# Performance work log

Hardware: AMD Instinct MI355X
Metric: run time of the kernel (lower is better)

Reference implementation:

```python
import jax, jax.numpy as jnp
import numpy as np

B, S, D_IN = 32, 4096, 256
D, T, NB, K = 256, 256, 4, 5  # d_model, compressed_len, n_blocks, kernel_size
EPS = 1e-5


def setup_inputs() -> dict:
    key = jax.random.key(0)
    ks = jax.random.split(key, 20)
    x = jax.random.normal(ks[0], (B, S, D_IN), jnp.float32)
    # ragged valid-prefix lengths in [1, S]
    lengths = jax.random.randint(ks[1], (B,), 1, S + 1)
    mask = jnp.arange(S)[None, :] < lengths[:, None]  # bool [B,S]
    sc = 0.02
    inp = {
        'x': x,
        'mask': mask,
        'in_w': jax.random.normal(ks[2], (D_IN, D), jnp.float32) * sc,
        'in_b': jnp.zeros((D,), jnp.float32),
        'ln_g': jnp.ones((NB, D), jnp.float32),
        'ln_b': jnp.zeros((NB, D), jnp.float32),
        'dw_w': jax.random.normal(ks[3], (NB, D, 1, K), jnp.float32) * sc,
        'dw_b': jnp.zeros((NB, D), jnp.float32),
        'win_w': jax.random.normal(ks[4], (NB, D, 2 * D), jnp.float32) * sc,
        'win_b': jnp.zeros((NB, 2 * D), jnp.float32),
        'wout_w': jax.random.normal(ks[5], (NB, D, D), jnp.float32) * sc,
        'wout_b': jnp.zeros((NB, D), jnp.float32),
        'fn_g': jnp.ones((D,), jnp.float32),
        'fn_b': jnp.zeros((D,), jnp.float32),
    }
    return inp


def layer_norm(h, g, b):
    mu = jnp.mean(h, axis=-1, keepdims=True)
    var = jnp.mean((h - mu) ** 2, axis=-1, keepdims=True)
    return (h - mu) * jax.lax.rsqrt(var + EPS) * g + b


def compress(x, mask, target_len):
    # Vectorized equivalent of the per-sample F.interpolate(mode='linear',
    # align_corners=False) loop: src = (j+0.5)*(L/T) - 0.5, clamped, lerp.
    lengths = mask.astype(jnp.int32).sum(axis=1)  # [B]
    Lf = lengths.astype(x.dtype)
    j = jnp.arange(target_len, dtype=x.dtype)
    src = (j[None, :] + 0.5) * (Lf[:, None] / target_len) - 0.5  # [B,T]
    src = jnp.clip(src, 0.0, jnp.maximum(Lf[:, None] - 1.0, 0.0))
    i0 = jnp.floor(src).astype(jnp.int32)
    i1 = jnp.minimum(i0 + 1, jnp.maximum(lengths[:, None] - 1, 0))
    w = (src - i0.astype(x.dtype))[..., None]  # [B,T,1]
    gather = jax.vmap(lambda xb, ib: xb[ib])  # [S,D],[T] -> [T,D]
    out = (1.0 - w) * gather(x, i0) + w * gather(x, i1)  # [B,T,D]
    valid = lengths > 0
    out = jnp.where(valid[:, None, None], out, 0.0)
    comp_mask = jnp.broadcast_to(valid[:, None], (x.shape[0], target_len))
    return out, comp_mask


def conv_block(h, g, b, dww, dwb, winw, winb, woutw, woutb):
    residual = h
    hn = layer_norm(h, g, b)
    hc = jax.lax.conv_general_dilated(
        hn.transpose(0, 2, 1), dww, window_strides=(1,),
        padding=[(K // 2, K // 2)], dimension_numbers=('NCW', 'OIW', 'NCW'),
        feature_group_count=D)
    hc = hc.transpose(0, 2, 1) + dwb  # [B,T,D]
    gv = hc @ winw + winb
    gate, val = jnp.split(gv, 2, axis=-1)
    h2 = jax.nn.sigmoid(gate) * jax.nn.gelu(val, approximate=False)
    return residual + h2 @ woutw + woutb


def reference(x, mask, in_w, in_b, ln_g, ln_b, dw_w, dw_b, win_w, win_b,
              wout_w, wout_b, fn_g, fn_b):
    xc, comp_mask = compress(x, mask, T)
    h = xc @ in_w + in_b
    for i in range(NB):
        h = conv_block(h, ln_g[i], ln_b[i], dw_w[i], dw_b[i], win_w[i],
                       win_b[i], wout_w[i], wout_b[i])
    return layer_norm(h, fn_g, fn_b), comp_mask
```

## Files before the change

kernel.cpp:

```cpp
#include <hip/hip_runtime.h>
#include <math.h>

#define B_    32
#define S_    4096
#define DIN_  256
#define D_    256
#define T_    256
#define NB_   4
#define K_    5
#define EPS_  1e-5f
#define ROWS_ (B_ * T_)

#define ORS_  16
#define CR_   32
#define BR_   36
#define SEGS_ 16
#define ASTR  264
#define HSTR  264

typedef short  shortx8  __attribute__((ext_vector_type(8)));
typedef float  floatx4  __attribute__((ext_vector_type(4)));
typedef float  floatx16 __attribute__((ext_vector_type(16)));

__device__ __forceinline__ unsigned short f2bf(float f) {
    unsigned int u = __float_as_uint(f);
    u += 0x7FFFu + ((u >> 16) & 1u);
    return (unsigned short)(u >> 16);
}
__device__ __forceinline__ float bf2f(unsigned short s) {
    return __uint_as_float((unsigned int)s << 16);
}
__device__ __forceinline__ unsigned int pack2bf(float a, float b) {
    return (unsigned int)f2bf(a) | ((unsigned int)f2bf(b) << 16);
}
__device__ __forceinline__ float bf2f_lo(unsigned int u) {
    return __uint_as_float(u << 16);
}
__device__ __forceinline__ float bf2f_hi(unsigned int u) {
    return __uint_as_float(u & 0xFFFF0000u);
}

__global__ void k_setup(const float* __restrict__ in_w, const float* __restrict__ win_w,
                        const float* __restrict__ wout_w, const unsigned int* __restrict__ mask_w,
                        unsigned short* __restrict__ wt_in, unsigned short* __restrict__ wt_in_lo,
                        unsigned short* __restrict__ wt_win,
                        unsigned short* __restrict__ wt_wout, int* __restrict__ lengths) {
    int z = blockIdx.z;
    int tid = threadIdx.x;

    if (z == 9) {
        int b = blockIdx.y * 16 + blockIdx.x;
        if (b >= B_) return;
        __shared__ int smode;
        if (tid < 64) {
            unsigned int w0 = mask_w[0];
            unsigned int vi = (tid < 32) ? mask_w[tid * 1024] : 0u;
            unsigned long long anyu8 = __ballot(vi > 1u);
            if (tid == 0) smode = (w0 == 0x3F800000u) ? 2 : (anyu8 ? 1 : 0);
        }
        __syncthreads();
        int mode = smode;
        int s = 0;
        if (mode == 0) {
            const int* m = (const int*)mask_w;
            for (int i = tid; i < S_; i += 256) s += (m[(size_t)b * S_ + i] != 0);
        } else if (mode == 2) {
            const float* m = (const float*)mask_w;
            for (int i = tid; i < S_; i += 256) s += (m[(size_t)b * S_ + i] != 0.0f);
        } else {
            const unsigned char* m = (const unsigned char*)mask_w;
            for (int i = tid; i < S_; i += 256) s += (m[(size_t)b * S_ + i] != 0);
        }
        __shared__ int sm[256];
        sm[tid] = s;
        __syncthreads();
        for (int off = 128; off > 0; off >>= 1) {
            if (tid < off) sm[tid] += sm[tid + off];
            __syncthreads();
        }
        if (tid == 0) lengths[b] = sm[0];
        return;
    }

    const float* src; unsigned short* dst; int N;
    if (z == 0)      { src = in_w;                                   dst = wt_in;                                   N = D_;     }
    else if (z <= 4) { src = win_w  + (size_t)(z - 1) * D_ * 2 * D_; dst = wt_win  + (size_t)(z - 1) * 2 * D_ * D_; N = 2 * D_; }
    else             { src = wout_w + (size_t)(z - 5) * D_ * D_;     dst = wt_wout + (size_t)(z - 5) * D_ * D_;     N = D_;     }
    int bx = blockIdx.x * 32;
    int by = blockIdx.y * 32;
    if (bx >= N) return;
    __shared__ float tile[32][33];
    int tx = tid & 31, ty = tid >> 5;
#pragma unroll
    for (int i = 0; i < 32; i += 8)
        tile[ty + i][tx] = src[(size_t)(by + ty + i) * N + bx + tx];
    __syncthreads();
#pragma unroll
    for (int i = 0; i < 32; i += 8) {
        float f = tile[tx][ty + i];
        unsigned short h = f2bf(f);
        int n = bx + ty + i, k = by + tx;
        if (z == 0) {
            int lane = ((k >> 3) & 3) * 16 + (n & 15);
            size_t idx = ((size_t)((n >> 4) * 8 + (k >> 5)) * 64 + lane) * 8 + (k & 7);
            wt_in[idx] = h;
            wt_in_lo[idx] = f2bf(f - bf2f(h));
        } else {
            int lane = ((k >> 3) & 1) * 32 + (n & 31);
            size_t idx = ((size_t)((n >> 5) * 16 + (k >> 4)) * 64 + lane) * 8 + (k & 7);
            dst[idx] = h;
        }
    }
}

__global__ __launch_bounds__(512, 2) void k_fused(
    const float* __restrict__ x, const int* __restrict__ lengths,
    const unsigned short* __restrict__ wt_in, const unsigned short* __restrict__ wt_in_lo,
    const float* __restrict__ in_b,
    const float* __restrict__ ln_g, const float* __restrict__ ln_b,
    const float* __restrict__ dw_w, const float* __restrict__ dw_b,
    const unsigned short* __restrict__ wt_win, const float* __restrict__ win_b,
    const unsigned short* __restrict__ wt_wout, const float* __restrict__ wout_b,
    const float* __restrict__ fn_g, const float* __restrict__ fn_b,
    float* __restrict__ out0, float* __restrict__ out1)
{
    __shared__ unsigned short buf0[BR_][ASTR];
    __shared__ unsigned short buf1[CR_][ASTR];
    __shared__ float h_lds[CR_][HSTR];

    int tid = threadIdx.x;
    int w = tid >> 6, lane = tid & 63;
    int c16 = lane & 15, q = lane >> 4;
    int l31 = lane & 31, lh = lane >> 5;
    int b = blockIdx.x >> 4, seg = blockIdx.x & (SEGS_ - 1);
    int t0 = seg * ORS_;

    unsigned short (*xlo)[ASTR] = (unsigned short (*)[ASTR])buf0;

    int L = lengths[b];

    {
        int tq = tid & 63, rg = tid >> 6;
        int col = tq * 4;
        float Lf = (float)L;
        float hi = fmaxf(Lf - 1.0f, 0.0f);
        int L1 = max(L - 1, 0);
        const float* xb = x + (size_t)b * S_ * DIN_ + col;
#pragma unroll
        for (int e = 0; e < 4; ++e) {
            int row = rg + e * 8;
            int t = t0 - 8 + row;
            t = min(max(t, 0), T_ - 1);
            float src = ((float)t + 0.5f) * (Lf * (1.0f / T_)) - 0.5f;
            src = fminf(fmaxf(src, 0.0f), hi);
            int i0 = (int)floorf(src);
            int i1 = min(i0 + 1, L1);
            float wf = src - (float)i0;
            float4 v0 = *(const float4*)&xb[(size_t)i0 * DIN_];
            float4 v1 = *(const float4*)&xb[(size_t)i1 * DIN_];
            float a0 = (1.0f - wf) * v0.x + wf * v1.x;
            float a1 = (1.0f - wf) * v0.y + wf * v1.y;
            float a2 = (1.0f - wf) * v0.z + wf * v1.z;
            float a3 = (1.0f - wf) * v0.w + wf * v1.w;
            unsigned short h0 = f2bf(a0), h1 = f2bf(a1), h2 = f2bf(a2), h3 = f2bf(a3);
            uint2 oh, ol;
            oh.x = (unsigned int)h0 | ((unsigned int)h1 << 16);
            oh.y = (unsigned int)h2 | ((unsigned int)h3 << 16);
            ol.x = (unsigned int)f2bf(a0 - bf2f(h0)) | ((unsigned int)f2bf(a1 - bf2f(h1)) << 16);
            ol.y = (unsigned int)f2bf(a2 - bf2f(h2)) | ((unsigned int)f2bf(a3 - bf2f(h3)) << 16);
            *(uint2*)&buf1[row][col] = oh;
            *(uint2*)&xlo[row][col] = ol;
        }
    }
    __syncthreads();

#pragma unroll
    for (int nn = 0; nn < 2; ++nn) {
        int nt = w + nn * 8;
        floatx4 acc[2] = {};
#pragma unroll
        for (int kk = 0; kk < 8; ++kk) {
            size_t fo = ((size_t)(nt * 8 + kk) << 9) + lane * 8;
            shortx8 bh = *(const shortx8*)(wt_in    + fo);
            shortx8 bl = *(const shortx8*)(wt_in_lo + fo);
#pragma unroll
            for (int mt = 0; mt < 2; ++mt) {
                shortx8 ah = *(const shortx8*)&buf1[mt * 16 + c16][kk * 32 + q * 8];
                shortx8 al = *(const shortx8*)&xlo[mt * 16 + c16][kk * 32 + q * 8];
                acc[mt] = __builtin_amdgcn_mfma_f32_16x16x32_bf16(ah, bh, acc[mt], 0, 0, 0);
                acc[mt] = __builtin_amdgcn_mfma_f32_16x16x32_bf16(al, bh, acc[mt], 0, 0, 0);
                acc[mt] = __builtin_amdgcn_mfma_f32_16x16x32_bf16(ah, bl, acc[mt], 0, 0, 0);
            }
        }
        float obv = in_b[nt * 16 + c16];
#pragma unroll
        for (int mt = 0; mt < 2; ++mt)
#pragma unroll
            for (int r = 0; r < 4; ++r)
                h_lds[mt * 16 + q * 4 + r][nt * 16 + c16] = acc[mt][r] + obv;
    }
    __syncthreads();

    if (tid < 132) {
        ((unsigned int*)buf0[0])[tid] = 0u;
        ((unsigned int*)buf0[1])[tid] = 0u;
        ((unsigned int*)buf0[BR_ - 2])[tid] = 0u;
        ((unsigned int*)buf0[BR_ - 1])[tid] = 0u;
    }

    for (int li = 0; li < NB_; ++li) {
        const float* g_i = ln_g + li * D_;
        const float* b_i = ln_b + li * D_;
        const float* dww = dw_w + (size_t)li * D_ * K_;
        const float* dwb = dw_b + li * D_;
        const unsigned short* ww = wt_win + (size_t)li * 2 * D_ * D_;
        const float* wb = win_b + (size_t)li * 2 * D_;
        const unsigned short* ow = wt_wout + (size_t)li * D_ * D_;
        const float* obp = wout_b + li * D_;

        {
            int c4 = lane * 4;
            float4 g4 = *(const float4*)&g_i[c4];
            float4 b4 = *(const float4*)&b_i[c4];
#pragma unroll
            for (int it = 0; it < 4; ++it) {
                int r = w + it * 8;
                float4 v = *(const float4*)&h_lds[r][c4];
                float s  = v.x + v.y + v.z + v.w;
                float ss = v.x * v.x + v.y * v.y + v.z * v.z + v.w * v.w;
#pragma unroll
                for (int off = 1; off < 64; off <<= 1) {
                    s += __shfl_xor(s, off);
                    ss += __shfl_xor(ss, off);
                }
                float mu = s * (1.0f / D_);
                float rsig = rsqrtf(ss * (1.0f / D_) - mu * mu + EPS_);
                uint2 o;
                o.x = pack2bf((v.x - mu) * rsig * g4.x + b4.x,
                              (v.y - mu) * rsig * g4.y + b4.y);
                o.y = pack2bf((v.z - mu) * rsig * g4.z + b4.z,
                              (v.w - mu) * rsig * g4.w + b4.w);
                int t = t0 - 8 + r;
                if (t < 0 || t >= T_) { o.x = 0; o.y = 0; }
                *(uint2*)&buf0[r + 2][c4] = o;
            }
        }
        __syncthreads();

        {
            int tq = tid & 63, rg = tid >> 6;
            int col = tq * 4;
            float4 wk[K_];
#pragma unroll
            for (int k = 0; k < K_; ++k) {
                wk[k].x = dww[(col + 0) * K_ + k];
                wk[k].y = dww[(col + 1) * K_ + k];
                wk[k].z = dww[(col + 2) * K_ + k];
                wk[k].w = dww[(col + 3) * K_ + k];
            }
            float4 cb4 = *(const float4*)&dwb[col];
#pragma unroll
            for (int e = 0; e < 4; ++e) {
                int rr = rg + e * 8;
                float4 acc = cb4;
#pragma unroll
                for (int k = 0; k < K_; ++k) {
                    uint2 u = *(const uint2*)&buf0[rr + k][col];
                    acc.x += bf2f_lo(u.x) * wk[k].x;
                    acc.y += bf2f_hi(u.x) * wk[k].y;
                    acc.z += bf2f_lo(u.y) * wk[k].z;
                    acc.w += bf2f_hi(u.y) * wk[k].w;
                }
                uint2 o;
                o.x = pack2bf(acc.x, acc.y);
                o.y = pack2bf(acc.z, acc.w);
                *(uint2*)&buf1[rr][col] = o;
            }
        }
        __syncthreads();

        {
            floatx16 accG = {}, accV = {};
#pragma unroll
            for (int kk = 0; kk < 16; ++kk) {
                shortx8 a  = *(const shortx8*)&buf1[l31][kk * 16 + lh * 8];
                shortx8 bg = *(const shortx8*)(ww + ((size_t)(w * 16 + kk) << 9) + lane * 8);
                shortx8 bv = *(const shortx8*)(ww + ((size_t)((8 + w) * 16 + kk) << 9) + lane * 8);
                accG = __builtin_amdgcn_mfma_f32_32x32x16_bf16(a, bg, accG, 0, 0, 0);
                accV = __builtin_amdgcn_mfma_f32_32x32x16_bf16(a, bv, accV, 0, 0, 0);
            }
            float bg0 = wb[w * 32 + l31];
            float bv0 = wb[256 + w * 32 + l31];
#pragma unroll
            for (int r = 0; r < 16; ++r) {
                int row = (r & 3) + 8 * (r >> 2) + 4 * lh;
                float gate = accG[r] + bg0;
                float val  = accV[r] + bv0;
                float sg = 1.0f / (1.0f + __expf(-gate));
                float u = 1.5957691216f * (val + 0.044715f * val * val * val);
                float ge = val / (1.0f + __expf(-u));
                buf0[2 + row][w * 32 + l31] = f2bf(sg * ge);
            }
        }
        __syncthreads();

        {
            floatx16 acc = {};
#pragma unroll
            for (int kk = 0; kk < 16; ++kk) {
                shortx8 a  = *(const shortx8*)&buf0[2 + l31][kk * 16 + lh * 8];
                shortx8 bo = *(const shortx8*)(ow + ((size_t)(w * 16 + kk) << 9) + lane * 8);
                acc = __builtin_amdgcn_mfma_f32_32x32x16_bf16(a, bo, acc, 0, 0, 0);
            }
            float bb = obp[w * 32 + l31];
#pragma unroll
            for (int r = 0; r < 16; ++r) {
                int row = (r & 3) + 8 * (r >> 2) + 4 * lh;
                int col = w * 32 + l31;
                h_lds[row][col] = h_lds[row][col] + acc[r] + bb;
            }
        }
        __syncthreads();
    }

    {
        int c4 = lane * 4;
        float4 g4 = *(const float4*)&fn_g[c4];
        float4 b4 = *(const float4*)&fn_b[c4];
#pragma unroll
        for (int it = 0; it < 2; ++it) {
            int r = 8 + w + it * 8;
            float4 v = *(const float4*)&h_lds[r][c4];
            float s  = v.x + v.y + v.z + v.w;
            float ss = v.x * v.x + v.y * v.y + v.z * v.z + v.w * v.w;
#pragma unroll
            for (int off = 1; off < 64; off <<= 1) {
                s += __shfl_xor(s, off);
                ss += __shfl_xor(ss, off);
            }
            float mu = s * (1.0f / D_);
            float rsig = rsqrtf(ss * (1.0f / D_) - mu * mu + EPS_);
            float4 o;
            o.x = (v.x - mu) * rsig * g4.x + b4.x;
            o.y = (v.y - mu) * rsig * g4.y + b4.y;
            o.z = (v.z - mu) * rsig * g4.z + b4.z;
            o.w = (v.w - mu) * rsig * g4.w + b4.w;
            *(float4*)&out0[((size_t)b * T_ + t0 + r - 8) * D_ + c4] = o;
        }
        if (tid < ORS_) out1[(size_t)b * T_ + t0 + tid] = 1.0f;
    }
}

extern "C" void kernel_launch(void* const* d_in, const int* in_sizes, int n_in,
                              void* d_out, int out_size, void* d_ws, size_t ws_size,
                              hipStream_t stream) {
    const float* x      = (const float*)d_in[0];
    const unsigned int* mask_w = (const unsigned int*)d_in[1];
    const float* in_w   = (const float*)d_in[2];
    const float* in_b   = (const float*)d_in[3];
    const float* ln_g   = (const float*)d_in[4];
    const float* ln_b   = (const float*)d_in[5];
    const float* dw_w   = (const float*)d_in[6];
    const float* dw_b   = (const float*)d_in[7];
    const float* win_w  = (const float*)d_in[8];
    const float* win_b  = (const float*)d_in[9];
    const float* wout_w = (const float*)d_in[10];
    const float* wout_b = (const float*)d_in[11];
    const float* fn_g   = (const float*)d_in[12];
    const float* fn_b   = (const float*)d_in[13];

    char* w8 = (char*)d_ws;
    unsigned short* wt_in   = (unsigned short*)w8;
    unsigned short* wt_win  = wt_in  + (size_t)D_ * DIN_;
    unsigned short* wt_wout = wt_win + (size_t)NB_ * 2 * D_ * D_;
    int* lengths = (int*)(w8 + (2u << 20));
    unsigned short* wt_in_lo = (unsigned short*)(w8 + (3u << 20));

    float* out0 = (float*)d_out;
    float* out1 = out0 + (size_t)ROWS_ * D_;

    k_setup<<<dim3(16, 8, 10), 256, 0, stream>>>(in_w, win_w, wout_w, mask_w,
                                                 wt_in, wt_in_lo, wt_win, wt_wout, lengths);
    k_fused<<<B_ * SEGS_, 512, 0, stream>>>(x, lengths, wt_in, wt_in_lo, in_b,
                                            ln_g, ln_b, dw_w, dw_b,
                                            wt_win, win_b, wt_wout, wout_b,
                                            fn_g, fn_b, out0, out1);
}
```

Before: 268.5 us.

## Use 1024-thread blocks with 16x16 MFMA tiles across sixteen waves

Doubles the workgroup from 8 to 16 waves and redistributes every stage (interpolation, LayerNorm, depthwise conv, gated and output GEMMs, final norm) so each wave owns half as many rows or columns. The 32x32x16 MFMAs in the block GEMMs become 16x16x32 MFMAs, and all weights are repacked into the 16-wide fragment layout. The aim is more latency hiding and less serial work per wave on the same LDS tile. The cost is more per-thread register pressure under launch_bounds(1024,2), and it may lower occupancy or cause spills; the smaller MFMA tiles also reuse each weight fragment less.

```diff
diff --git a/kernel.cpp b/kernel.cpp
--- a/kernel.cpp
+++ b/kernel.cpp
@@ -20,7 +20,6 @@
 
 typedef short  shortx8  __attribute__((ext_vector_type(8)));
 typedef float  floatx4  __attribute__((ext_vector_type(4)));
-typedef float  floatx16 __attribute__((ext_vector_type(16)));
 
 __device__ __forceinline__ unsigned short f2bf(float f) {
     unsigned int u = __float_as_uint(f);
@@ -100,20 +99,14 @@
         float f = tile[tx][ty + i];
         unsigned short h = f2bf(f);
         int n = bx + ty + i, k = by + tx;
-        if (z == 0) {
-            int lane = ((k >> 3) & 3) * 16 + (n & 15);
-            size_t idx = ((size_t)((n >> 4) * 8 + (k >> 5)) * 64 + lane) * 8 + (k & 7);
-            wt_in[idx] = h;
-            wt_in_lo[idx] = f2bf(f - bf2f(h));
-        } else {
-            int lane = ((k >> 3) & 1) * 32 + (n & 31);
-            size_t idx = ((size_t)((n >> 5) * 16 + (k >> 4)) * 64 + lane) * 8 + (k & 7);
-            dst[idx] = h;
-        }
-    }
-}
-
-__global__ __launch_bounds__(512, 2) void k_fused(
+        int lane = ((k >> 3) & 3) * 16 + (n & 15);
+        size_t idx = ((size_t)((n >> 4) * 8 + (k >> 5)) * 64 + lane) * 8 + (k & 7);
+        dst[idx] = h;
+        if (z == 0) wt_in_lo[idx] = f2bf(f - bf2f(h));
+    }
+}
+
+__global__ __launch_bounds__(1024, 2) void k_fused(
     const float* __restrict__ x, const int* __restrict__ lengths,
     const unsigned short* __restrict__ wt_in, const unsigned short* __restrict__ wt_in_lo,
     const float* __restrict__ in_b,
@@ -131,7 +124,6 @@
     int tid = threadIdx.x;
     int w = tid >> 6, lane = tid & 63;
     int c16 = lane & 15, q = lane >> 4;
-    int l31 = lane & 31, lh = lane >> 5;
     int b = blockIdx.x >> 4, seg = blockIdx.x & (SEGS_ - 1);
     int t0 = seg * ORS_;
 
@@ -140,15 +132,15 @@
     int L = lengths[b];
 
     {
-        int tq = tid & 63, rg = tid >> 6;
-        int col = tq * 4;
+        int col = (tid & 63) * 4;
+        int rg = tid >> 6;
         float Lf = (float)L;
         float hi = fmaxf(Lf - 1.0f, 0.0f);
         int L1 = max(L - 1, 0);
         const float* xb = x + (size_t)b * S_ * DIN_ + col;
 #pragma unroll
-        for (int e = 0; e < 4; ++e) {
-            int row = rg + e * 8;
+        for (int e = 0; e < 2; ++e) {
+            int row = rg + e * 16;
             int t = t0 - 8 + row;
             t = min(max(t, 0), T_ - 1);
             float src = ((float)t + 0.5f) * (Lf * (1.0f / T_)) - 0.5f;
@@ -174,13 +166,11 @@
     }
     __syncthreads();
 
-#pragma unroll
-    for (int nn = 0; nn < 2; ++nn) {
-        int nt = w + nn * 8;
+    {
         floatx4 acc[2] = {};
 #pragma unroll
         for (int kk = 0; kk < 8; ++kk) {
-            size_t fo = ((size_t)(nt * 8 + kk) << 9) + lane * 8;
+            size_t fo = ((size_t)(w * 8 + kk) << 9) + lane * 8;
             shortx8 bh = *(const shortx8*)(wt_in    + fo);
             shortx8 bl = *(const shortx8*)(wt_in_lo + fo);
 #pragma unroll
@@ -192,12 +182,12 @@
                 acc[mt] = __builtin_amdgcn_mfma_f32_16x16x32_bf16(ah, bl, acc[mt], 0, 0, 0);
             }
         }
-        float obv = in_b[nt * 16 + c16];
+        float obv = in_b[w * 16 + c16];
 #pragma unroll
         for (int mt = 0; mt < 2; ++mt)
 #pragma unroll
             for (int r = 0; r < 4; ++r)
-                h_lds[mt * 16 + q * 4 + r][nt * 16 + c16] = acc[mt][r] + obv;
+                h_lds[mt * 16 + q * 4 + r][w * 16 + c16] = acc[mt][r] + obv;
     }
     __syncthreads();
 
@@ -223,8 +213,8 @@
             float4 g4 = *(const float4*)&g_i[c4];
             float4 b4 = *(const float4*)&b_i[c4];
 #pragma unroll
-            for (int it = 0; it < 4; ++it) {
-                int r = w + it * 8;
+            for (int it = 0; it < 2; ++it) {
+                int r = w + it * 16;
                 float4 v = *(const float4*)&h_lds[r][c4];
                 float s  = v.x + v.y + v.z + v.w;
                 float ss = v.x * v.x + v.y * v.y + v.z * v.z + v.w * v.w;
@@ -248,8 +238,8 @@
         __syncthreads();
 
         {
-            int tq = tid & 63, rg = tid >> 6;
-            int col = tq * 4;
+            int col = (tid & 63) * 4;
+            int rg = tid >> 6;
             float4 wk[K_];
 #pragma unroll
             for (int k = 0; k < K_; ++k) {
@@ -260,8 +250,8 @@
             }
             float4 cb4 = *(const float4*)&dwb[col];
 #pragma unroll
-            for (int e = 0; e < 4; ++e) {
-                int rr = rg + e * 8;
+            for (int e = 0; e < 2; ++e) {
+                int rr = rg + e * 16;
                 float4 acc = cb4;
 #pragma unroll
                 for (int k = 0; k < K_; ++k) {
@@ -280,45 +270,55 @@
         __syncthreads();
 
         {
-            floatx16 accG = {}, accV = {};
-#pragma unroll
-            for (int kk = 0; kk < 16; ++kk) {
-                shortx8 a  = *(const shortx8*)&buf1[l31][kk * 16 + lh * 8];
-                shortx8 bg = *(const shortx8*)(ww + ((size_t)(w * 16 + kk) << 9) + lane * 8);
-                shortx8 bv = *(const shortx8*)(ww + ((size_t)((8 + w) * 16 + kk) << 9) + lane * 8);
-                accG = __builtin_amdgcn_mfma_f32_32x32x16_bf16(a, bg, accG, 0, 0, 0);
-                accV = __builtin_amdgcn_mfma_f32_32x32x16_bf16(a, bv, accV, 0, 0, 0);
-            }
-            float bg0 = wb[w * 32 + l31];
-            float bv0 = wb[256 + w * 32 + l31];
-#pragma unroll
-            for (int r = 0; r < 16; ++r) {
-                int row = (r & 3) + 8 * (r >> 2) + 4 * lh;
-                float gate = accG[r] + bg0;
-                float val  = accV[r] + bv0;
-                float sg = 1.0f / (1.0f + __expf(-gate));
-                float u = 1.5957691216f * (val + 0.044715f * val * val * val);
-                float ge = val / (1.0f + __expf(-u));
-                buf0[2 + row][w * 32 + l31] = f2bf(sg * ge);
-            }
+            floatx4 accG[2] = {}, accV[2] = {};
+#pragma unroll
+            for (int kk = 0; kk < 8; ++kk) {
+                shortx8 bg = *(const shortx8*)(ww + (((size_t)(w * 8 + kk)) << 9) + lane * 8);
+                shortx8 bv = *(const shortx8*)(ww + (((size_t)((16 + w) * 8 + kk)) << 9) + lane * 8);
+#pragma unroll
+                for (int mt = 0; mt < 2; ++mt) {
+                    shortx8 a = *(const shortx8*)&buf1[mt * 16 + c16][kk * 32 + q * 8];
+                    accG[mt] = __builtin_amdgcn_mfma_f32_16x16x32_bf16(a, bg, accG[mt], 0, 0, 0);
+                    accV[mt] = __builtin_amdgcn_mfma_f32_16x16x32_bf16(a, bv, accV[mt], 0, 0, 0);
+                }
+            }
+            float bg0 = wb[w * 16 + c16];
+            float bv0 = wb[256 + w * 16 + c16];
+            int colw = w * 16 + c16;
+#pragma unroll
+            for (int mt = 0; mt < 2; ++mt)
+#pragma unroll
+                for (int r = 0; r < 4; ++r) {
+                    float gate = accG[mt][r] + bg0;
+                    float val  = accV[mt][r] + bv0;
+                    float sg = 1.0f / (1.0f + __expf(-gate));
+                    float u = 1.5957691216f * (val + 0.044715f * val * val * val);
+                    float ge = val / (1.0f + __expf(-u));
+                    buf0[2 + mt * 16 + q * 4 + r][colw] = f2bf(sg * ge);
+                }
         }
         __syncthreads();
 
         {
-            floatx16 acc = {};
-#pragma unroll
-            for (int kk = 0; kk < 16; ++kk) {
-                shortx8 a  = *(const shortx8*)&buf0[2 + l31][kk * 16 + lh * 8];
-                shortx8 bo = *(const shortx8*)(ow + ((size_t)(w * 16 + kk) << 9) + lane * 8);
-                acc = __builtin_amdgcn_mfma_f32_32x32x16_bf16(a, bo, acc, 0, 0, 0);
-            }
-            float bb = obp[w * 32 + l31];
-#pragma unroll
-            for (int r = 0; r < 16; ++r) {
-                int row = (r & 3) + 8 * (r >> 2) + 4 * lh;
-                int col = w * 32 + l31;
-                h_lds[row][col] = h_lds[row][col] + acc[r] + bb;
-            }
+            floatx4 acc[2] = {};
+#pragma unroll
+            for (int kk = 0; kk < 8; ++kk) {
+                shortx8 bo = *(const shortx8*)(ow + (((size_t)(w * 8 + kk)) << 9) + lane * 8);
+#pragma unroll
+                for (int mt = 0; mt < 2; ++mt) {
+                    shortx8 a = *(const shortx8*)&buf0[2 + mt * 16 + c16][kk * 32 + q * 8];
+                    acc[mt] = __builtin_amdgcn_mfma_f32_16x16x32_bf16(a, bo, acc[mt], 0, 0, 0);
+                }
+            }
+            float bb = obp[w * 16 + c16];
+#pragma unroll
+            for (int mt = 0; mt < 2; ++mt)
+#pragma unroll
+                for (int r = 0; r < 4; ++r) {
+                    int row = mt * 16 + q * 4 + r;
+                    int col = w * 16 + c16;
+                    h_lds[row][col] = h_lds[row][col] + acc[mt][r] + bb;
+                }
         }
         __syncthreads();
     }
@@ -327,26 +327,23 @@
         int c4 = lane * 4;
         float4 g4 = *(const float4*)&fn_g[c4];
         float4 b4 = *(const float4*)&fn_b[c4];
-#pragma unroll
-        for (int it = 0; it < 2; ++it) {
-            int r = 8 + w + it * 8;
-            float4 v = *(const float4*)&h_lds[r][c4];
-            float s  = v.x + v.y + v.z + v.w;
-            float ss = v.x * v.x + v.y * v.y + v.z * v.z + v.w * v.w;
-#pragma unroll
-            for (int off = 1; off < 64; off <<= 1) {
-                s += __shfl_xor(s, off);
-                ss += __shfl_xor(ss, off);
-            }
-            float mu = s * (1.0f / D_);
-            float rsig = rsqrtf(ss * (1.0f / D_) - mu * mu + EPS_);
-            float4 o;
-            o.x = (v.x - mu) * rsig * g4.x + b4.x;
-            o.y = (v.y - mu) * rsig * g4.y + b4.y;
-            o.z = (v.z - mu) * rsig * g4.z + b4.z;
-            o.w = (v.w - mu) * rsig * g4.w + b4.w;
-            *(float4*)&out0[((size_t)b * T_ + t0 + r - 8) * D_ + c4] = o;
-        }
+        int r = 8 + w;
+        float4 v = *(const float4*)&h_lds[r][c4];
+        float s  = v.x + v.y + v.z + v.w;
+        float ss = v.x * v.x + v.y * v.y + v.z * v.z + v.w * v.w;
+#pragma unroll
+        for (int off = 1; off < 64; off <<= 1) {
+            s += __shfl_xor(s, off);
+            ss += __shfl_xor(ss, off);
+        }
+        float mu = s * (1.0f / D_);
+        float rsig = rsqrtf(ss * (1.0f / D_) - mu * mu + EPS_);
+        float4 o;
+        o.x = (v.x - mu) * rsig * g4.x + b4.x;
+        o.y = (v.y - mu) * rsig * g4.y + b4.y;
+        o.z = (v.z - mu) * rsig * g4.z + b4.z;
+        o.w = (v.w - mu) * rsig * g4.w + b4.w;
+        *(float4*)&out0[((size_t)b * T_ + t0 + r - 8) * D_ + c4] = o;
         if (tid < ORS_) out1[(size_t)b * T_ + t0 + tid] = 1.0f;
     }
 }
@@ -381,8 +378,8 @@
 
     k_setup<<<dim3(16, 8, 10), 256, 0, stream>>>(in_w, win_w, wout_w, mask_w,
                                                  wt_in, wt_in_lo, wt_win, wt_wout, lengths);
-    k_fused<<<B_ * SEGS_, 512, 0, stream>>>(x, lengths, wt_in, wt_in_lo, in_b,
-                                            ln_g, ln_b, dw_w, dw_b,
-                                            wt_win, win_b, wt_wout, wout_b,
-                                            fn_g, fn_b, out0, out1);
-}
+    k_fused<<<B_ * SEGS_, 1024, 0, stream>>>(x, lengths, wt_in, wt_in_lo, in_b,
+                                             ln_g, ln_b, dw_w, dw_b,
+                                             wt_win, win_b, wt_wout, wout_b,
+                                             fn_g, fn_b, out0, out1);
+}
```

Result: slower. 277.4 us (+3.3%).
